# Performance work log

Hardware: AMD Instinct MI355X
Metric: run time of the kernel (lower is better)

Reference implementation:

```python
import jax, jax.numpy as jnp
import numpy as np

DIM = 768
H = 12
HD = DIM // H
LN_EPS = 1e-5


def setup_inputs() -> dict:
    key = jax.random.key(0)
    ks = jax.random.split(key, 8)
    B, N, C = 64, 197, DIM
    s = 0.02
    return {
        "x": jax.random.normal(ks[0], (B, N, C), jnp.float32),
        "qkv_w": jax.random.normal(ks[1], (C, 3 * C), jnp.float32) * s,
        "qkv_b": jnp.zeros((3 * C,), jnp.float32),
        "proj_w": jax.random.normal(ks[2], (C, C), jnp.float32) * s,
        "proj_b": jnp.zeros((C,), jnp.float32),
        "ht_w": jax.random.normal(ks[3], (HD, C), jnp.float32) * s,
        "ht_b": jnp.zeros((C,), jnp.float32),
        "ln_g": jnp.ones((HD,), jnp.float32),
        "ln_b": jnp.zeros((HD,), jnp.float32),
        "pos_embed": jax.random.normal(ks[4], (1, H, C), jnp.float32) * s,
    }


def reference(x, qkv_w, qkv_b, proj_w, proj_b, ht_w, ht_b, ln_g, ln_b, pos_embed):
    B, N, C = x.shape
    scale = HD ** -0.5
    # head tokens: mean over sequence per head -> [B, H, HD]
    ht = x.reshape(B, N, H, HD).mean(axis=1)
    ht = ht @ ht_w + ht_b                      # [B, H, C]
    ht = ht.reshape(B, H, H, HD)
    mu = ht.mean(axis=-1, keepdims=True)
    var = jnp.mean((ht - mu) ** 2, axis=-1, keepdims=True)
    ht = (ht - mu) * jax.lax.rsqrt(var + LN_EPS) * ln_g + ln_b
    ht = jax.nn.gelu(ht, approximate=False).reshape(B, H, C) + pos_embed
    xc = jnp.concatenate([x, ht], axis=1)      # [B, T=N+H, C]
    T = N + H
    qkv = (xc @ qkv_w + qkv_b).reshape(B, T, 3, H, HD)
    q, k, v = qkv[:, :, 0], qkv[:, :, 1], qkv[:, :, 2]  # [B, T, H, HD]
    attn = jnp.einsum('bqhd,bkhd->bhqk', q, k) * scale
    attn = jax.nn.softmax(attn, axis=-1)
    out = jnp.einsum('bhqk,bkhd->bqhd', attn, v).reshape(B, T, C)
    out = out @ proj_w + proj_b
    cls = out[:, :1] + out[:, N:].mean(axis=1, keepdims=True)
    return jnp.concatenate([cls, out[:, 1:N]], axis=1)
```

## Files before the change

### kernel.cpp

```cpp
#include <hip/hip_runtime.h>
#include <cstdint>
#include <cstddef>

typedef unsigned short u16;
typedef __attribute__((ext_vector_type(8))) __bf16 bf16x8;
typedef __attribute__((ext_vector_type(4))) unsigned short u16x4;
typedef __attribute__((ext_vector_type(4))) float f32x4;

#define NTOK 197
#define TT   209
#define CDIM 768
#define NH   12
#define HD   64
#define BATCH 64
#define GM (BATCH*TT)
#define VTP 224
#define NQKV 2304
#define XN (BATCH*NTOK*CDIM)

__device__ __forceinline__ float bf2f(u16 u){ return __uint_as_float(((unsigned)u)<<16); }
__device__ __forceinline__ u16 f2bf(float f){
  unsigned x = __float_as_uint(f);
  return (u16)((x + 0x7FFFu + ((x>>16)&1u)) >> 16);
}

__device__ __forceinline__ void gll16(const void* g, void* l){
  __builtin_amdgcn_global_load_lds((const __attribute__((address_space(1))) void*)g,
                                   (__attribute__((address_space(3))) void*)l,
                                   16, 0, 0);
}

__device__ __forceinline__ float wsum64(float v){
  #pragma unroll
  for (int o = 32; o > 0; o >>= 1) v += __shfl_xor(v, o, 64);
  return v;
}

__device__ __forceinline__ int detect_f(const u16* __restrict__ x){
  const int lane = threadIdx.x & 63;
  float mx = 0.f;
  #pragma unroll
  for (int i = 0; i < 16; i++) {
    float v = fabsf(bf2f(x[i*64 + lane]));
    if (!(v < 1e30f)) v = 1e30f;
    mx = fmaxf(mx, v);
  }
  #pragma unroll
  for (int o = 32; o; o >>= 1) mx = fmaxf(mx, __shfl_xor(mx, o, 64));
  return mx < 1e5f;
}

__device__ __forceinline__ float ldany(const void* p, size_t i, int f){
  return f ? bf2f(((const u16*)p)[i]) : ((const float*)p)[i];
}

__global__ __launch_bounds__(256) void prep_kernel(
    const void* __restrict__ xr, const void* __restrict__ w1, const void* __restrict__ w2,
    const void* __restrict__ htw, const void* __restrict__ htb,
    const void* __restrict__ lng, const void* __restrict__ lnb, const void* __restrict__ pos,
    const void* __restrict__ qb_raw, const void* __restrict__ pb_raw,
    u16* __restrict__ xc, u16* __restrict__ o1, u16* __restrict__ o2,
    u16* __restrict__ ht, u16* __restrict__ qbb, u16* __restrict__ pbb,
    int* __restrict__ flagp)
{
  const int tid = threadIdx.x;
  const int f = detect_f((const u16*)xr);
  const int bid = blockIdx.x;
  __shared__ u16 lds[64][66];
  __shared__ float part[4][64];
  __shared__ float msh[64];

  if (bid >= 1600) {
    if (bid == 1600) {
      if (tid == 0) *flagp = f;
      for (int i = tid; i < NQKV; i += 256) qbb[i] = f2bf(ldany(qb_raw, i, f));
    } else {
      for (int i = tid; i < CDIM; i += 256) pbb[i] = f2bf(ldany(pb_raw, i, f));
    }
    return;
  }
  if (bid < 256) {
    if (f) return;
    const f32x4* in = (const f32x4*)xr;
    const int n4 = XN >> 2;
    for (int i = bid*256 + tid; i < n4; i += 256*256) {
      f32x4 v = in[i];
      u16x4 o;
      #pragma unroll
      for (int j=0;j<4;j++) o[j] = f2bf(v[j]);
      ((u16x4*)xc)[i] = o;
    }
    return;
  }
  if (bid < 832) {
    const void* in; u16* out; int N, tx, ty;
    if (bid < 688) { int t = bid-256; in = w1; out = o1; N = NQKV; tx = t % 36; ty = t / 36; }
    else           { int t = bid-688; in = w2; out = o2; N = CDIM; tx = t % 12; ty = t / 12; }
    const int n0 = tx*64, k0 = ty*64;
    const int c = tid & 63, r0 = tid >> 6;
    #pragma unroll
    for (int i=0;i<16;i++) {
      int r = i*4 + r0;
      size_t idx = (size_t)(k0+r)*N + n0 + c;
      lds[r][c] = f ? ((const u16*)in)[idx] : f2bf(((const float*)in)[idx]);
    }
    __syncthreads();
    #pragma unroll
    for (int i=0;i<16;i++) {
      int r = i*4 + r0;
      out[(size_t)(n0+r)*CDIM + k0 + c] = lds[c][r];
    }
    return;
  }

  const int idx = bid - 832;
  const int b = idx / NH, h = idx - b*NH;
  const int c = tid & 63, rg = tid >> 6;
  float s = 0.f;
  for (int n = rg; n < NTOK; n += 4)
    s += ldany(xr, (size_t)(b*NTOK + n)*CDIM + h*HD + c, f);
  part[rg][c] = s;
  __syncthreads();
  if (tid < 64) msh[tid] = (part[0][tid]+part[1][tid]+part[2][tid]+part[3][tid]) * (1.0f/(float)NTOK);
  __syncthreads();

  float v0 = ldany(htb, tid, f), v1 = ldany(htb, tid+256, f), v2 = ldany(htb, tid+512, f);
  for (int d = 0; d < HD; d++) {
    const float md = msh[d];
    const size_t wr = (size_t)d*CDIM;
    v0 += md * ldany(htw, wr + tid, f);
    v1 += md * ldany(htw, wr + tid + 256, f);
    v2 += md * ldany(htw, wr + tid + 512, f);
  }
  const float gam = ldany(lng, tid & 63, f), bet = ldany(lnb, tid & 63, f);
  float vv[3] = {v0, v1, v2};
  #pragma unroll
  for (int ch = 0; ch < 3; ch++) {
    int cc = ch*256 + tid;
    float mu = wsum64(vv[ch]) * (1.0f/(float)HD);
    float dv = vv[ch] - mu;
    float var = wsum64(dv*dv) * (1.0f/(float)HD);
    float y = dv * rsqrtf(var + 1e-5f) * gam + bet;
    float ge = 0.5f * y * (1.0f + erff(y * 0.70710678118654752f));
    float o = ge + ldany(pos, h*CDIM + cc, f);
    ht[((size_t)(b*NH + h))*CDIM + cc] = f2bf(o);
  }
}

template<int MODE>
__global__ __launch_bounds__(256, 2) void gemm_kernel(
    const u16* __restrict__ A0c, const void* __restrict__ A0r,
    const u16* __restrict__ A1,
    const u16* __restrict__ Bt, const u16* __restrict__ bias,
    u16* __restrict__ qout,
    void* __restrict__ outv, float* __restrict__ csb, const int* __restrict__ flag)
{
  const int tid = threadIdx.x;
  const int lane = tid & 63;
  const int w = tid >> 6;
  const int wm = w >> 1, wn = w & 1;
  const int lr = lane & 15, kg = lane >> 4;

  const int NT = gridDim.x;
  const int nwg = NT * gridDim.y;
  const int orig = blockIdx.y * NT + blockIdx.x;
  const int xcd = orig & 7, sIdx = orig >> 3;
  const int q = nwg >> 3, r = nwg & 7;
  const int wg = ((xcd < r) ? xcd*(q+1) : r*(q+1) + (xcd-r)*q) + sIdx;
  const int tm = wg / NT, tn = wg - tm*NT;

  __shared__ __align__(16) u16 As[5][4096];
  __shared__ __align__(16) u16 Bs[5][4096];

  const int f = *flag;
  const u16* A0 = (MODE == 0) ? (f ? (const u16*)A0r : A0c) : A0c;

  f32x4 acc[4][4];
  #pragma unroll
  for (int i=0;i<4;i++)
    #pragma unroll
    for (int j=0;j<4;j++) acc[i][j] = (f32x4){0.f,0.f,0.f,0.f};

  const u16* garow[2];
  const u16* gbrow[2];
  #pragma unroll
  for (int i=0;i<2;i++){
    int row = (i*4 + w)*16 + (lane >> 2);
    int rr = tm*128 + row; if (rr > GM-1) rr = GM-1;
    if (MODE == 0) {
      int bb = rr / TT; int t = rr - bb*TT;
      garow[i] = (t < NTOK) ? (A0 + (size_t)(bb*NTOK + t)*CDIM)
                            : (A1 + (size_t)(bb*NH + (t - NTOK))*CDIM);
    } else {
      garow[i] = A0 + (size_t)rr*CDIM;
    }
    gbrow[i] = Bt + (size_t)(tn*128 + row)*CDIM;
  }
  const int gseg = (lane & 3) ^ ((lane >> 3) & 3);

#define STAGE(kt_, bf_) do { \
    const int ko_ = (kt_)*32 + gseg*8; \
    gll16(garow[0] + ko_, (void*)&As[bf_][(0*4+w)*512]); \
    gll16(garow[1] + ko_, (void*)&As[bf_][(1*4+w)*512]); \
    gll16(gbrow[0] + ko_, (void*)&Bs[bf_][(0*4+w)*512]); \
    gll16(gbrow[1] + ko_, (void*)&Bs[bf_][(1*4+w)*512]); \
  } while(0)

  STAGE(0, 0);
  STAGE(1, 1);
  STAGE(2, 2);

  const int spA = kg ^ ((lr >> 1) & 3);

  #pragma unroll
  for (int kt = 0; kt < 24; kt++) {
    const int cb = kt % 5;
    if (kt < 21) {
      STAGE(kt+3, (kt+3)%5);
      asm volatile("s_waitcnt vmcnt(12)" ::: "memory");
    } else if (kt == 21) {
      asm volatile("s_waitcnt vmcnt(8)" ::: "memory");
    } else if (kt == 22) {
      asm volatile("s_waitcnt vmcnt(4)" ::: "memory");
    } else {
      asm volatile("s_waitcnt vmcnt(0)" ::: "memory");
    }
    __builtin_amdgcn_s_barrier();

    bf16x8 av[4], bv[4];
    #pragma unroll
    for (int mi=0; mi<4; mi++)
      av[mi] = *(const bf16x8*)&As[cb][(wm*64+mi*16+lr)*32 + spA*8];
    #pragma unroll
    for (int ni=0; ni<4; ni++)
      bv[ni] = *(const bf16x8*)&Bs[cb][(wn*64+ni*16+lr)*32 + spA*8];
    #pragma unroll
    for (int mi=0; mi<4; mi++)
      #pragma unroll
      for (int ni=0; ni<4; ni++)
        acc[mi][ni] = __builtin_amdgcn_mfma_f32_16x16x32_bf16(av[mi], bv[ni], acc[mi][ni], 0,0,0);
  }
#undef STAGE

  #pragma unroll
  for (int mi=0; mi<4; mi++){
    const int rb = tm*128 + wm*64 + mi*16 + kg*4;
    #pragma unroll
    for (int ni=0; ni<4; ni++){
      const int c = tn*128 + wn*64 + ni*16 + lr;
      const float bs = bf2f(bias[c]);
      if (MODE == 0) {
        #pragma unroll
        for (int j=0;j<4;j++){
          int rr = rb + j;
          if (rr < GM) qout[(size_t)rr*NQKV + c] = f2bf(acc[mi][ni][j] + bs);
        }
      } else {
        #pragma unroll
        for (int j=0;j<4;j++){
          int rr = rb + j;
          if (rr < GM) {
            int bb = rr / TT; int t = rr - bb*TT;
            float v = acc[mi][ni][j] + bs;
            if (t >= 1 && t < NTOK) {
              size_t oi = ((size_t)(bb*NTOK + t))*CDIM + c;
              if (f) ((u16*)outv)[oi] = f2bf(v);
              else   ((float*)outv)[oi] = v;
            } else {
              int idx = (t == 0) ? 0 : (t - NTOK + 1);
              csb[((size_t)(bb*13 + idx))*CDIM + c] = v;
            }
          }
        }
      }
    }
  }
}

__global__ __launch_bounds__(256) void vtrans_kernel(
    const u16* __restrict__ qkvo, u16* __restrict__ vb)
{
  __shared__ u16 lds[64][66];
  const int tt0 = blockIdx.x*64;
  const int bh = blockIdx.y;
  const int b = bh / NH, h = bh - b*NH;
  const int c = threadIdx.x & 63, r0 = threadIdx.x >> 6;
  #pragma unroll
  for (int i=0;i<16;i++) {
    int t = tt0 + i*4 + r0;
    u16 v = 0;
    if (t < TT) v = qkvo[(size_t)(b*TT + t)*NQKV + 1536 + h*64 + c];
    lds[i*4+r0][c] = v;
  }
  __syncthreads();
  #pragma unroll
  for (int i=0;i<16;i++) {
    int d = i*4 + r0;
    int t = tt0 + c;
    if (t < VTP) vb[((size_t)(bh)*HD + d)*VTP + t] = lds[c][d];
  }
}

__global__ __launch_bounds__(256) void attn_kernel(
    const u16* __restrict__ qkvo, const u16* __restrict__ vt, u16* __restrict__ ob)
{
  __shared__ __align__(16) u16 Kl[224*72];
  __shared__ __align__(16) u16 P[4][7*16*32];
  const int tid = threadIdx.x;
  const int lane = tid & 63;
  const int w = tid >> 6;
  const int lr = lane & 15, kg = lane >> 4;

  const int bh = blockIdx.x;
  const int b = bh / NH, h = bh - b*NH;

  const u16* qg  = qkvo + (size_t)(b*TT)*NQKV + h*64;
  const u16* kgp = qg + CDIM;
  const u16* vg  = vt + (size_t)bh*HD*VTP;

  for (int s = tid; s < 224*8; s += 256) {
    int kc = s >> 3, seg = s & 7;
    uint4 val = make_uint4(0,0,0,0);
    if (kc < TT) val = *(const uint4*)&kgp[(size_t)kc*NQKV + seg*8];
    *(uint4*)&Kl[kc*72 + seg*8] = val;
  }
  __syncthreads();

  u16* Pw = &P[w][0];
  for (int ck = w; ck < 14; ck += 4) {
    const int q0 = ck*16;
    int qrow = q0 + lr; if (qrow > TT-1) qrow = TT-1;
    const bf16x8 qf0 = *(const bf16x8*)&qg[(size_t)qrow*NQKV + kg*8];
    const bf16x8 qf1 = *(const bf16x8*)&qg[(size_t)qrow*NQKV + 32 + kg*8];

    f32x4 sv[14];
    #pragma unroll
    for (int kt = 0; kt < 14; kt++) {
      bf16x8 kf0 = *(const bf16x8*)&Kl[(kt*16+lr)*72 + kg*8];
      bf16x8 kf1 = *(const bf16x8*)&Kl[(kt*16+lr)*72 + 32 + kg*8];
      f32x4 sa = {0.f,0.f,0.f,0.f};
      sa = __builtin_amdgcn_mfma_f32_16x16x32_bf16(kf0, qf0, sa, 0,0,0);
      sa = __builtin_amdgcn_mfma_f32_16x16x32_bf16(kf1, qf1, sa, 0,0,0);
      sv[kt] = sa;
    }

    float m = -3.0e38f;
    #pragma unroll
    for (int kt = 0; kt < 13; kt++)
      #pragma unroll
      for (int j=0;j<4;j++){ sv[kt][j] *= 0.125f; m = fmaxf(m, sv[kt][j]); }
    #pragma unroll
    for (int j=0;j<4;j++){
      sv[13][j] *= 0.125f;
      if (208 + kg*4 + j < TT) m = fmaxf(m, sv[13][j]);
    }
    m = fmaxf(m, __shfl_xor(m, 16, 64));
    m = fmaxf(m, __shfl_xor(m, 32, 64));

    float ssum = 0.f;
    #pragma unroll
    for (int kt = 0; kt < 13; kt++)
      #pragma unroll
      for (int j=0;j<4;j++){ float e = __expf(sv[kt][j] - m); sv[kt][j] = e; ssum += e; }
    #pragma unroll
    for (int j=0;j<4;j++){
      float e = (208 + kg*4 + j < TT) ? __expf(sv[13][j] - m) : 0.f;
      sv[13][j] = e; ssum += e;
    }
    ssum += __shfl_xor(ssum, 16, 64);
    ssum += __shfl_xor(ssum, 32, 64);
    const float inv = 1.0f / ssum;

    #pragma unroll
    for (int kt = 0; kt < 14; kt++) {
      u16x4 pk;
      #pragma unroll
      for (int j=0;j<4;j++) pk[j] = f2bf(sv[kt][j] * inv);
      *(u16x4*)&Pw[(kt>>1)*512 + lr*32 + (kt&1)*16 + kg*4] = pk;
    }

    f32x4 acc[4];
    #pragma unroll
    for (int dt=0; dt<4; dt++) acc[dt] = (f32x4){0.f,0.f,0.f,0.f};
    #pragma unroll
    for (int ks = 0; ks < 7; ks++) {
      bf16x8 pf = *(const bf16x8*)&Pw[ks*512 + lr*32 + kg*8];
      #pragma unroll
      for (int dt = 0; dt < 4; dt++) {
        bf16x8 vf = *(const bf16x8*)&vg[(dt*16+lr)*VTP + ks*32 + kg*8];
        acc[dt] = __builtin_amdgcn_mfma_f32_16x16x32_bf16(pf, vf, acc[dt], 0,0,0);
      }
    }

    #pragma unroll
    for (int dt = 0; dt < 4; dt++)
      #pragma unroll
      for (int j = 0; j < 4; j++) {
        int tq = q0 + kg*4 + j;
        if (tq < TT)
          ob[((size_t)(b*TT + tq))*CDIM + h*HD + dt*16 + lr] = f2bf(acc[dt][j]);
      }
  }
}

__global__ __launch_bounds__(256) void final2_kernel(
    const float* __restrict__ csb, void* __restrict__ outv, const int* __restrict__ flag)
{
  const int f = *flag;
  int i = blockIdx.x*256 + threadIdx.x;
  if (i >= BATCH*CDIM) return;
  int b = i / CDIM, c = i - b*CDIM;
  const float* p = csb + (size_t)b*13*CDIM + c;
  float s = 0.f;
  #pragma unroll
  for (int j = 1; j <= 12; j++) s += p[(size_t)j*CDIM];
  float v = p[0] + s * (1.0f/12.0f);
  size_t oi = ((size_t)b*NTOK)*CDIM + c;
  if (f) ((u16*)outv)[oi] = f2bf(v);
  else   ((float*)outv)[oi] = v;
}

extern "C" void kernel_launch(void* const* d_in, const int* in_sizes, int n_in,
                              void* d_out, int out_size, void* d_ws, size_t ws_size,
                              hipStream_t stream)
{
  char* ws = (char*)d_ws;
  size_t off = 0;
  auto alloc = [&](size_t bytes)->void* {
    void* p = ws + off; off += (bytes + 255) & ~(size_t)255; return p;
  };

  int* flag  = (int*)alloc(256);
  u16* qbb   = (u16*)alloc((size_t)NQKV*2);
  u16* pbb   = (u16*)alloc((size_t)CDIM*2);
  u16* xconv = (u16*)alloc((size_t)XN*2);
  u16* qkvT  = (u16*)alloc((size_t)3*CDIM*CDIM*2);
  u16* projT = (u16*)alloc((size_t)CDIM*CDIM*2);
  u16* htb_  = (u16*)alloc((size_t)BATCH*NH*CDIM*2);
  u16* qkvo  = (u16*)alloc((size_t)GM*NQKV*2);
  u16* vb    = (u16*)alloc((size_t)BATCH*NH*HD*VTP*2);
  float* csb = (float*)alloc((size_t)BATCH*13*CDIM*4);
  u16* ao    = xconv;

  prep_kernel<<<1602, 256, 0, stream>>>(
      d_in[0], d_in[1], d_in[3], d_in[5], d_in[6], d_in[7], d_in[8], d_in[9],
      d_in[2], d_in[4],
      xconv, qkvT, projT, htb_, qbb, pbb, flag);
  gemm_kernel<0><<<dim3(NQKV/128, (GM+127)/128), 256, 0, stream>>>(
      xconv, d_in[0], htb_, qkvT, qbb, qkvo, nullptr, nullptr, flag);
  vtrans_kernel<<<dim3(4, BATCH*NH), 256, 0, stream>>>(qkvo, vb);
  attn_kernel<<<BATCH*NH, 256, 0, stream>>>(qkvo, vb, ao);
  gemm_kernel<1><<<dim3(CDIM/128, (GM+127)/128), 256, 0, stream>>>(
      ao, nullptr, nullptr, projT, pbb, nullptr, d_out, csb, flag);
  final2_kernel<<<(BATCH*CDIM+255)/256, 256, 0, stream>>>(csb, d_out, flag);
}
```

Before: 217.8 us.

## Fuse V transpose into attention kernel via LDS staging

```diff
diff --git a/kernel.cpp b/kernel.cpp
--- a/kernel.cpp
+++ b/kernel.cpp
@@ -277,35 +277,12 @@
   }
 }
 
-__global__ __launch_bounds__(256) void vtrans_kernel(
-    const u16* __restrict__ qkvo, u16* __restrict__ vb)
-{
-  __shared__ u16 lds[64][66];
-  const int tt0 = blockIdx.x*64;
-  const int bh = blockIdx.y;
-  const int b = bh / NH, h = bh - b*NH;
-  const int c = threadIdx.x & 63, r0 = threadIdx.x >> 6;
-  #pragma unroll
-  for (int i=0;i<16;i++) {
-    int t = tt0 + i*4 + r0;
-    u16 v = 0;
-    if (t < TT) v = qkvo[(size_t)(b*TT + t)*NQKV + 1536 + h*64 + c];
-    lds[i*4+r0][c] = v;
-  }
-  __syncthreads();
-  #pragma unroll
-  for (int i=0;i<16;i++) {
-    int d = i*4 + r0;
-    int t = tt0 + c;
-    if (t < VTP) vb[((size_t)(bh)*HD + d)*VTP + t] = lds[c][d];
-  }
-}
-
 __global__ __launch_bounds__(256) void attn_kernel(
-    const u16* __restrict__ qkvo, const u16* __restrict__ vt, u16* __restrict__ ob)
+    const u16* __restrict__ qkvo, u16* __restrict__ ob)
 {
   __shared__ __align__(16) u16 Kl[224*72];
-  __shared__ __align__(16) u16 P[4][7*16*32];
+  __shared__ __align__(16) u16 Vt[64*232];
+  __shared__ __align__(16) u16 P[4][16*32];
   const int tid = threadIdx.x;
   const int lane = tid & 63;
   const int w = tid >> 6;
@@ -314,15 +291,23 @@
   const int bh = blockIdx.x;
   const int b = bh / NH, h = bh - b*NH;
 
-  const u16* qg  = qkvo + (size_t)(b*TT)*NQKV + h*64;
-  const u16* kgp = qg + CDIM;
-  const u16* vg  = vt + (size_t)bh*HD*VTP;
+  const u16* qg   = qkvo + (size_t)(b*TT)*NQKV + h*64;
+  const u16* kgp  = qg + CDIM;
+  const u16* vsrc = qg + 2*CDIM;
 
   for (int s = tid; s < 224*8; s += 256) {
     int kc = s >> 3, seg = s & 7;
     uint4 val = make_uint4(0,0,0,0);
     if (kc < TT) val = *(const uint4*)&kgp[(size_t)kc*NQKV + seg*8];
     *(uint4*)&Kl[kc*72 + seg*8] = val;
+  }
+  for (int s = tid; s < TT*64; s += 256) {
+    int t = s >> 6, d = s & 63;
+    Vt[d*232 + t] = vsrc[(size_t)t*NQKV + d];
+  }
+  for (int s = tid; s < 64*(VTP-TT); s += 256) {
+    int d = s / (VTP-TT), i = s - d*(VTP-TT);
+    Vt[d*232 + TT + i] = 0;
   }
   __syncthreads();
 
@@ -371,23 +356,23 @@
     ssum += __shfl_xor(ssum, 32, 64);
     const float inv = 1.0f / ssum;
 
-    #pragma unroll
-    for (int kt = 0; kt < 14; kt++) {
-      u16x4 pk;
-      #pragma unroll
-      for (int j=0;j<4;j++) pk[j] = f2bf(sv[kt][j] * inv);
-      *(u16x4*)&Pw[(kt>>1)*512 + lr*32 + (kt&1)*16 + kg*4] = pk;
-    }
-
     f32x4 acc[4];
     #pragma unroll
     for (int dt=0; dt<4; dt++) acc[dt] = (f32x4){0.f,0.f,0.f,0.f};
     #pragma unroll
     for (int ks = 0; ks < 7; ks++) {
-      bf16x8 pf = *(const bf16x8*)&Pw[ks*512 + lr*32 + kg*8];
+      u16x4 pk0, pk1;
+      #pragma unroll
+      for (int j=0;j<4;j++){
+        pk0[j] = f2bf(sv[2*ks  ][j] * inv);
+        pk1[j] = f2bf(sv[2*ks+1][j] * inv);
+      }
+      *(u16x4*)&Pw[lr*32      + kg*4] = pk0;
+      *(u16x4*)&Pw[lr*32 + 16 + kg*4] = pk1;
+      bf16x8 pf = *(const bf16x8*)&Pw[lr*32 + kg*8];
       #pragma unroll
       for (int dt = 0; dt < 4; dt++) {
-        bf16x8 vf = *(const bf16x8*)&vg[(dt*16+lr)*VTP + ks*32 + kg*8];
+        bf16x8 vf = *(const bf16x8*)&Vt[(dt*16+lr)*232 + ks*32 + kg*8];
         acc[dt] = __builtin_amdgcn_mfma_f32_16x16x32_bf16(pf, vf, acc[dt], 0,0,0);
       }
     }
@@ -438,7 +423,6 @@
   u16* projT = (u16*)alloc((size_t)CDIM*CDIM*2);
   u16* htb_  = (u16*)alloc((size_t)BATCH*NH*CDIM*2);
   u16* qkvo  = (u16*)alloc((size_t)GM*NQKV*2);
-  u16* vb    = (u16*)alloc((size_t)BATCH*NH*HD*VTP*2);
   float* csb = (float*)alloc((size_t)BATCH*13*CDIM*4);
   u16* ao    = xconv;
 
@@ -448,8 +432,7 @@
       xconv, qkvT, projT, htb_, qbb, pbb, flag);
   gemm_kernel<0><<<dim3(NQKV/128, (GM+127)/128), 256, 0, stream>>>(
       xconv, d_in[0], htb_, qkvT, qbb, qkvo, nullptr, nullptr, flag);
-  vtrans_kernel<<<dim3(4, BATCH*NH), 256, 0, stream>>>(qkvo, vb);
-  attn_kernel<<<BATCH*NH, 256, 0, stream>>>(qkvo, vb, ao);
+  attn_kernel<<<BATCH*NH, 256, 0, stream>>>(qkvo, ao);
   gemm_kernel<1><<<dim3(CDIM/128, (GM+127)/128), 256, 0, stream>>>(
       ao, nullptr, nullptr, projT, pbb, nullptr, d_out, csb, flag);
   final2_kernel<<<(BATCH*CDIM+255)/256, 256, 0, stream>>>(csb, d_out, flag);
```

After: 211.8 us, median of 2. -2.8%, faster.
